# Kernel optimization log

Measured on AMD Instinct MI355X. Metric: run time of the kernel, lower is better.

The kernel has to match this reference:

```python
import jax, jax.numpy as jnp
import numpy as np

INNER_DIM = 64
NEG = 1e12


def _rotate_half_interleaved(x):
    # stack([-x[..., 1::2], x[..., ::2]], -1).reshape(x.shape)
    x2 = jnp.stack([-x[..., 1::2], x[..., ::2]], axis=-1)
    return x2.reshape(x.shape)


def setup_inputs() -> dict:
    key = jax.random.key(0)
    k1, k2 = jax.random.split(key)
    B, S, H = 16, 512, 768
    T, D = 9, INNER_DIM
    hidden = jax.random.normal(k1, (B, S, H), dtype=jnp.float32)
    W = jax.random.normal(k2, (H, T * 2 * D), dtype=jnp.float32) * 0.02
    b = jnp.zeros((T * 2 * D,), dtype=jnp.float32)
    attention_mask = jnp.ones((B, S), dtype=jnp.int32)
    return {"hidden": hidden, "W": W, "b": b, "attention_mask": attention_mask}


def reference(hidden, W, b, attention_mask):
    B, S, H = hidden.shape
    D = INNER_DIM
    T = W.shape[1] // (2 * D)

    # dense + split into per-type q/k: [B, S, T, 2D]
    out = (jnp.einsum('bsh,hc->bsc', hidden, W) + b).reshape(B, S, T, 2 * D)
    qw, kw = out[..., :D], out[..., D:]

    # inline sinusoidal RoPE (interleaved sin/cos layout)
    pos = jnp.arange(S, dtype=jnp.float32)[:, None]            # [S, 1]
    inv = jnp.power(10000.0, -2.0 * jnp.arange(D // 2, dtype=jnp.float32) / D)
    ang = pos * inv                                            # [S, D/2]
    cos_pos = jnp.repeat(jnp.cos(ang), 2, axis=-1)[None, :, None, :]  # [1,S,1,D]
    sin_pos = jnp.repeat(jnp.sin(ang), 2, axis=-1)[None, :, None, :]
    qw = qw * cos_pos + _rotate_half_interleaved(qw) * sin_pos
    kw = kw * cos_pos + _rotate_half_interleaved(kw) * sin_pos

    # pairwise scores per entity type: [B, T, S, S]
    logits = jnp.einsum('bmtd,bntd->btmn', qw, kw)

    # padding mask (key dim only, as in original expand) with large negative
    pm = attention_mask.astype(logits.dtype)[:, None, None, :]  # [B,1,1,S]
    logits = logits * pm - (1.0 - pm) * NEG

    # strict lower-triangular mask (only upper-triangular spans valid)
    tril = jnp.tril(jnp.ones((S, S), dtype=logits.dtype), -1)
    logits = logits - tril * NEG

    return logits / np.sqrt(D).astype(np.float32)
```

## Files before the change

kernel.cpp:

```cpp
#include <hip/hip_runtime.h>
#include <cstdint>
#include <cstddef>

#define NEG_C 1000000000000.0f

typedef __bf16 bf16x8 __attribute__((ext_vector_type(8)));
typedef float f32x4 __attribute__((ext_vector_type(4)));

union Frag {
    int4 i;
    bf16x8 b;
};

__device__ __forceinline__ unsigned short f32_to_bf16_rne(float f) {
    unsigned int u = __float_as_uint(f);
    u += 0x7fffu + ((u >> 16) & 1u);
    return (unsigned short)(u >> 16);
}

__device__ __forceinline__ void async_copy16(const void* g, void* l) {
    __builtin_amdgcn_global_load_lds(
        (const __attribute__((address_space(1))) unsigned int*)(uintptr_t)g,
        (__attribute__((address_space(3))) unsigned int*)(uintptr_t)l,
        16, 0, 0);
}

__global__ void prep_kernel(const float* __restrict__ W,
                            unsigned short* __restrict__ WT,
                            const float* __restrict__ hidden,
                            unsigned short* __restrict__ Ah) {
    __shared__ unsigned short tile[32][33];
    int blk = blockIdx.x;
    if (blk < 864) {
        int bx = blk % 36;
        int by = blk / 36;
        int x = threadIdx.x & 31;
        int y0 = threadIdx.x >> 5;
#pragma unroll
        for (int yy = 0; yy < 32; yy += 8) {
            int k = by * 32 + y0 + yy;
            int n = bx * 32 + x;
            tile[y0 + yy][x] = f32_to_bf16_rne(W[(size_t)k * 1152 + n]);
        }
        __syncthreads();
#pragma unroll
        for (int yy = 0; yy < 32; yy += 8) {
            int n = bx * 32 + y0 + yy;
            int k = by * 32 + x;
            WT[(size_t)n * 768 + k] = tile[x][y0 + yy];
        }
    } else {
        int idx = (blk - 864) * 256 + threadIdx.x;
        float4 v = ((const float4*)hidden)[idx];
        ushort4 o;
        o.x = f32_to_bf16_rne(v.x);
        o.y = f32_to_bf16_rne(v.y);
        o.z = f32_to_bf16_rne(v.z);
        o.w = f32_to_bf16_rne(v.w);
        ((ushort4*)Ah)[idx] = o;
    }
}

__global__ __launch_bounds__(256, 3) void gemm1_kernel(
    const unsigned short* __restrict__ Ah, const unsigned short* __restrict__ WT,
    const float* __restrict__ bias, unsigned short* __restrict__ proj) {
    const int K = 768, N = 1152;
    __shared__ unsigned short As[128 * 64];
    __shared__ unsigned short Bs[128 * 64];
    int tid = threadIdx.x;
    int lane = tid & 63;
    int wave = tid >> 6;
    int bm = blockIdx.y * 128;
    int bn = blockIdx.x * 128;
    int wm = (wave & 1) * 64;
    int wn = (wave >> 1) * 64;
    int col_l = lane & 15;
    int qg = lane >> 4;

    int c0 = wave * 4 * 64 + lane;
    f32x4 acc[4][4] = {};

    for (int k0 = 0; k0 < K; k0 += 64) {
        __syncthreads();
#pragma unroll
        for (int q = 0; q < 4; ++q) {
            int c = c0 + q * 64;
            int r = c >> 3;
            int g = (c & 7) ^ (r & 7);
            async_copy16(Ah + (size_t)(bm + r) * K + k0 + g * 8,
                         As + (size_t)(wave * 4 + q) * 512);
            async_copy16(WT + (size_t)(bn + r) * K + k0 + g * 8,
                         Bs + (size_t)(wave * 4 + q) * 512);
        }
        __syncthreads();
#pragma unroll
        for (int ks = 0; ks < 2; ++ks) {
            Frag qf[4], kf[4];
            int g = ks * 4 + qg;
#pragma unroll
            for (int i = 0; i < 4; ++i) {
                int rm = wm + i * 16 + col_l;
                int rn = wn + i * 16 + col_l;
                qf[i].i = *(const int4*)(As + rm * 64 + ((g ^ (rm & 7)) * 8));
                kf[i].i = *(const int4*)(Bs + rn * 64 + ((g ^ (rn & 7)) * 8));
            }
#pragma unroll
            for (int i = 0; i < 4; ++i)
#pragma unroll
                for (int j = 0; j < 4; ++j)
                    acc[i][j] = __builtin_amdgcn_mfma_f32_16x16x32_bf16(
                        kf[i].b, qf[j].b, acc[i][j], 0, 0, 0);
        }
    }

#pragma unroll
    for (int i = 0; i < 4; ++i) {
        int cn0 = wn + i * 16 + qg * 4;
        int gn0 = bn + cn0;
        float4 bb = *(const float4*)(bias + gn0);
        int p0 = (cn0 & 63) >> 1;
        float inv0 = exp2f(-0.41524101186091903f * (float)p0);
        float inv1 = exp2f(-0.41524101186091903f * (float)(p0 + 1));
#pragma unroll
        for (int j = 0; j < 4; ++j) {
            int gm = bm + wm + j * 16 + col_l;
            float s = (float)(gm & 511);
            float a0 = s * inv0, a1 = s * inv1;
            float sn0 = __sinf(a0), cs0 = __cosf(a0);
            float sn1 = __sinf(a1), cs1 = __cosf(a1);
            float v0 = acc[i][j][0] + bb.x;
            float v1 = acc[i][j][1] + bb.y;
            float v2 = acc[i][j][2] + bb.z;
            float v3 = acc[i][j][3] + bb.w;
            ushort4 o;
            o.x = f32_to_bf16_rne(v0 * cs0 - v1 * sn0);
            o.y = f32_to_bf16_rne(v1 * cs0 + v0 * sn0);
            o.z = f32_to_bf16_rne(v2 * cs1 - v3 * sn1);
            o.w = f32_to_bf16_rne(v3 * cs1 + v2 * sn1);
            *(ushort4*)(proj + (size_t)gm * N + gn0) = o;
        }
    }
}

__global__ __launch_bounds__(256, 3) void gemm2_kernel(
    const unsigned short* __restrict__ proj, const int* __restrict__ mask,
    float* __restrict__ out) {
    __shared__ unsigned short Qs[128 * 64];
    __shared__ unsigned short Ks[128 * 64];
    int bid = blockIdx.x;
    int batch = bid >> 4;
    int tl = bid & 15;
    int tm = tl >> 2, tn = tl & 3;
    int b = batch / 9, t = batch - b * 9;
    int tid = threadIdx.x, lane = tid & 63, wave = tid >> 6;
    int wm = (wave & 1) * 64, wn = (wave >> 1) * 64;
    int col_l = lane & 15;
    int qg = lane >> 4;
    size_t out_base = ((size_t)b * 9 + t) * 512 * 512;

    if (tm > tn) {
#pragma unroll 4
        for (int r = 0; r < 128; r += 8) {
            int row = r + (tid >> 5);
            int c4 = (tid & 31) * 4;
            int gm = tm * 128 + row;
            int gn = tn * 128 + c4;
            int4 mi = *(const int4*)(mask + b * 512 + gn);
            f32x4 v;
            v[0] = (-(1.0f - (float)mi.x) * NEG_C - NEG_C) * 0.125f;
            v[1] = (-(1.0f - (float)mi.y) * NEG_C - NEG_C) * 0.125f;
            v[2] = (-(1.0f - (float)mi.z) * NEG_C - NEG_C) * 0.125f;
            v[3] = (-(1.0f - (float)mi.w) * NEG_C - NEG_C) * 0.125f;
            *(f32x4*)(out + out_base + (size_t)gm * 512 + gn) = v;
        }
        return;
    }

    const unsigned short* qbase = proj + (((size_t)(b * 512 + tm * 128) * 9) + t) * 128;
    const unsigned short* kbase = proj + (((size_t)(b * 512 + tn * 128) * 9) + t) * 128 + 64;
#pragma unroll
    for (int q = 0; q < 4; ++q) {
        int c = (wave * 4 + q) * 64 + lane;
        int r = c >> 3;
        int g = (c & 7) ^ (r & 7);
        async_copy16(qbase + (size_t)r * 1152 + g * 8,
                     Qs + (size_t)(wave * 4 + q) * 512);
        async_copy16(kbase + (size_t)r * 1152 + g * 8,
                     Ks + (size_t)(wave * 4 + q) * 512);
    }
    __syncthreads();

    f32x4 acc[4][4] = {};
#pragma unroll
    for (int ks = 0; ks < 2; ++ks) {
        Frag qf[4], kf[4];
        int g = ks * 4 + qg;
#pragma unroll
        for (int i = 0; i < 4; ++i) {
            int rm = wm + i * 16 + col_l;
            int rn = wn + i * 16 + col_l;
            qf[i].i = *(const int4*)(Qs + rm * 64 + ((g ^ (rm & 7)) * 8));
            kf[i].i = *(const int4*)(Ks + rn * 64 + ((g ^ (rn & 7)) * 8));
        }
#pragma unroll
        for (int i = 0; i < 4; ++i)
#pragma unroll
            for (int j = 0; j < 4; ++j)
                acc[i][j] = __builtin_amdgcn_mfma_f32_16x16x32_bf16(
                    kf[i].b, qf[j].b, acc[i][j], 0, 0, 0);
    }

#pragma unroll
    for (int i = 0; i < 4; ++i) {
        int gn0 = tn * 128 + wn + i * 16 + qg * 4;
        int4 mi = *(const int4*)(mask + b * 512 + gn0);
#pragma unroll
        for (int j = 0; j < 4; ++j) {
            int gm = tm * 128 + wm + j * 16 + col_l;
            f32x4 v;
#pragma unroll
            for (int r = 0; r < 4; ++r) {
                float pm = (float)((&mi.x)[r]);
                float x = acc[i][j][r] * pm - (1.0f - pm) * NEG_C;
                if (gm > gn0 + r) x -= NEG_C;
                v[r] = x * 0.125f;
            }
            *(f32x4*)(out + out_base + (size_t)gm * 512 + gn0) = v;
        }
    }
}

extern "C" void kernel_launch(void* const* d_in, const int* in_sizes, int n_in,
                              void* d_out, int out_size, void* d_ws, size_t ws_size,
                              hipStream_t stream) {
    const float* hidden = (const float*)d_in[0];
    const float* W      = (const float*)d_in[1];
    const float* bias   = (const float*)d_in[2];
    const int*   mask   = (const int*)d_in[3];
    float* out = (float*)d_out;

    char* ws = (char*)d_ws;
    unsigned short* Ah   = (unsigned short*)(ws);
    unsigned short* WT   = (unsigned short*)(ws + 12582912);
    unsigned short* proj = (unsigned short*)(ws + 14352384);

    prep_kernel<<<7008, 256, 0, stream>>>(W, WT, hidden, Ah);
    dim3 g1(9, 64);
    gemm1_kernel<<<g1, 256, 0, stream>>>(Ah, WT, bias, proj);
    gemm2_kernel<<<2304, 256, 0, stream>>>(proj, mask, out);
}
```

Before: 214.3 us.

## Process a full row band per block with double-buffered K tiles in gemm2

gemm2 now launches one block per (batch, type, row tile). Each block loops over the upper-triangular column tiles, reusing the loaded Q tile and prefetching the next K tile into a second LDS buffer. The block also writes the masked lower-triangular tiles itself. This reduces the block count and redundant Q loads and overlaps K loads with MFMA work. The cost is uneven per-block work and fewer blocks in flight for a write-bound kernel.

```diff
diff --git a/kernel.cpp b/kernel.cpp
--- a/kernel.cpp
+++ b/kernel.cpp
@@ -146,24 +146,96 @@
     const unsigned short* __restrict__ proj, const int* __restrict__ mask,
     float* __restrict__ out) {
     __shared__ unsigned short Qs[128 * 64];
-    __shared__ unsigned short Ks[128 * 64];
+    __shared__ unsigned short Ks[2][128 * 64];
     int bid = blockIdx.x;
-    int batch = bid >> 4;
-    int tl = bid & 15;
-    int tm = tl >> 2, tn = tl & 3;
+    int tm = bid & 3;
+    int batch = bid >> 2;
     int b = batch / 9, t = batch - b * 9;
     int tid = threadIdx.x, lane = tid & 63, wave = tid >> 6;
     int wm = (wave & 1) * 64, wn = (wave >> 1) * 64;
     int col_l = lane & 15;
     int qg = lane >> 4;
-    size_t out_base = ((size_t)b * 9 + t) * 512 * 512;
-
-    if (tm > tn) {
-#pragma unroll 4
-        for (int r = 0; r < 128; r += 8) {
-            int row = r + (tid >> 5);
-            int c4 = (tid & 31) * 4;
-            int gm = tm * 128 + row;
+    size_t out_base = ((size_t)b * 9 + t) * (512 * 512);
+
+    {
+        const unsigned short* qbase =
+            proj + (((size_t)(b * 512 + tm * 128) * 9) + t) * 128;
+        const unsigned short* kbase = qbase + 64;
+#pragma unroll
+        for (int q = 0; q < 4; ++q) {
+            int c = (wave * 4 + q) * 64 + lane;
+            int r = c >> 3;
+            int g = (c & 7) ^ (r & 7);
+            async_copy16(qbase + (size_t)r * 1152 + g * 8,
+                         Qs + (size_t)(wave * 4 + q) * 512);
+            async_copy16(kbase + (size_t)r * 1152 + g * 8,
+                         Ks[0] + (size_t)(wave * 4 + q) * 512);
+        }
+    }
+    __syncthreads();
+
+    int cur = 0;
+    for (int tn = tm; tn < 4; ++tn) {
+        if (tn + 1 < 4) {
+            const unsigned short* kbase =
+                proj + (((size_t)(b * 512 + (tn + 1) * 128) * 9) + t) * 128 + 64;
+#pragma unroll
+            for (int q = 0; q < 4; ++q) {
+                int c = (wave * 4 + q) * 64 + lane;
+                int r = c >> 3;
+                int g = (c & 7) ^ (r & 7);
+                async_copy16(kbase + (size_t)r * 1152 + g * 8,
+                             Ks[cur ^ 1] + (size_t)(wave * 4 + q) * 512);
+            }
+        }
+
+        f32x4 acc[4][4] = {};
+#pragma unroll
+        for (int ks = 0; ks < 2; ++ks) {
+            Frag qf[4], kf[4];
+            int g = ks * 4 + qg;
+#pragma unroll
+            for (int i = 0; i < 4; ++i) {
+                int rm = wm + i * 16 + col_l;
+                int rn = wn + i * 16 + col_l;
+                qf[i].i = *(const int4*)(Qs + rm * 64 + ((g ^ (rm & 7)) * 8));
+                kf[i].i = *(const int4*)(Ks[cur] + rn * 64 + ((g ^ (rn & 7)) * 8));
+            }
+#pragma unroll
+            for (int i = 0; i < 4; ++i)
+#pragma unroll
+                for (int j = 0; j < 4; ++j)
+                    acc[i][j] = __builtin_amdgcn_mfma_f32_16x16x32_bf16(
+                        kf[i].b, qf[j].b, acc[i][j], 0, 0, 0);
+        }
+
+#pragma unroll
+        for (int i = 0; i < 4; ++i) {
+            int gn0 = tn * 128 + wn + i * 16 + qg * 4;
+            int4 mi = *(const int4*)(mask + b * 512 + gn0);
+#pragma unroll
+            for (int j = 0; j < 4; ++j) {
+                int gm = tm * 128 + wm + j * 16 + col_l;
+                f32x4 v;
+#pragma unroll
+                for (int r = 0; r < 4; ++r) {
+                    float pm = (float)((&mi.x)[r]);
+                    float x = acc[i][j][r] * pm - (1.0f - pm) * NEG_C;
+                    if (gm > gn0 + r) x -= NEG_C;
+                    v[r] = x * 0.125f;
+                }
+                *(f32x4*)(out + out_base + (size_t)gm * 512 + gn0) = v;
+            }
+        }
+
+        __syncthreads();
+        cur ^= 1;
+    }
+
+    {
+        int row = tid >> 5;
+        int c4 = (tid & 31) * 4;
+        for (int tn = 0; tn < tm; ++tn) {
             int gn = tn * 128 + c4;
             int4 mi = *(const int4*)(mask + b * 512 + gn);
             f32x4 v;
@@ -171,61 +243,11 @@
             v[1] = (-(1.0f - (float)mi.y) * NEG_C - NEG_C) * 0.125f;
             v[2] = (-(1.0f - (float)mi.z) * NEG_C - NEG_C) * 0.125f;
             v[3] = (-(1.0f - (float)mi.w) * NEG_C - NEG_C) * 0.125f;
-            *(f32x4*)(out + out_base + (size_t)gm * 512 + gn) = v;
-        }
-        return;
-    }
-
-    const unsigned short* qbase = proj + (((size_t)(b * 512 + tm * 128) * 9) + t) * 128;
-    const unsigned short* kbase = proj + (((size_t)(b * 512 + tn * 128) * 9) + t) * 128 + 64;
-#pragma unroll
-    for (int q = 0; q < 4; ++q) {
-        int c = (wave * 4 + q) * 64 + lane;
-        int r = c >> 3;
-        int g = (c & 7) ^ (r & 7);
-        async_copy16(qbase + (size_t)r * 1152 + g * 8,
-                     Qs + (size_t)(wave * 4 + q) * 512);
-        async_copy16(kbase + (size_t)r * 1152 + g * 8,
-                     Ks + (size_t)(wave * 4 + q) * 512);
-    }
-    __syncthreads();
-
-    f32x4 acc[4][4] = {};
-#pragma unroll
-    for (int ks = 0; ks < 2; ++ks) {
-        Frag qf[4], kf[4];
-        int g = ks * 4 + qg;
-#pragma unroll
-        for (int i = 0; i < 4; ++i) {
-            int rm = wm + i * 16 + col_l;
-            int rn = wn + i * 16 + col_l;
-            qf[i].i = *(const int4*)(Qs + rm * 64 + ((g ^ (rm & 7)) * 8));
-            kf[i].i = *(const int4*)(Ks + rn * 64 + ((g ^ (rn & 7)) * 8));
-        }
-#pragma unroll
-        for (int i = 0; i < 4; ++i)
-#pragma unroll
-            for (int j = 0; j < 4; ++j)
-                acc[i][j] = __builtin_amdgcn_mfma_f32_16x16x32_bf16(
-                    kf[i].b, qf[j].b, acc[i][j], 0, 0, 0);
-    }
-
-#pragma unroll
-    for (int i = 0; i < 4; ++i) {
-        int gn0 = tn * 128 + wn + i * 16 + qg * 4;
-        int4 mi = *(const int4*)(mask + b * 512 + gn0);
-#pragma unroll
-        for (int j = 0; j < 4; ++j) {
-            int gm = tm * 128 + wm + j * 16 + col_l;
-            f32x4 v;
-#pragma unroll
-            for (int r = 0; r < 4; ++r) {
-                float pm = (float)((&mi.x)[r]);
-                float x = acc[i][j][r] * pm - (1.0f - pm) * NEG_C;
-                if (gm > gn0 + r) x -= NEG_C;
-                v[r] = x * 0.125f;
-            }
-            *(f32x4*)(out + out_base + (size_t)gm * 512 + gn0) = v;
+#pragma unroll
+            for (int r8 = 0; r8 < 128; r8 += 8) {
+                int gm = tm * 128 + r8 + row;
+                *(f32x4*)(out + out_base + (size_t)gm * 512 + gn) = v;
+            }
         }
     }
 }
@@ -247,5 +269,5 @@
     prep_kernel<<<7008, 256, 0, stream>>>(W, WT, hidden, Ah);
     dim3 g1(9, 64);
     gemm1_kernel<<<g1, 256, 0, stream>>>(Ah, WT, bias, proj);
-    gemm2_kernel<<<2304, 256, 0, stream>>>(proj, mask, out);
-}
+    gemm2_kernel<<<576, 256, 0, stream>>>(proj, mask, out);
+}
```

New measurement: 224.4 us. +4.7%, slower.

## Double-buffer LDS tiles in projection GEMM to overlap loads with MFMA

Applied to the files above, without the earlier changes.

Gives the first GEMM two LDS buffers per operand and issues the async global-to-LDS copies for the next K slice before computing on the current one. This is meant to hide global load latency behind the MFMA work and removes one barrier per iteration. In exchange LDS use doubles to 64 KB per block and the occupancy hint drops from 3 to 2 blocks per CU. The gemm1 stage is only part of total time, which is dominated by the large fp32 output write in gemm2.

```diff
diff --git a/kernel.cpp b/kernel.cpp
--- a/kernel.cpp
+++ b/kernel.cpp
@@ -61,12 +61,12 @@
     }
 }
 
-__global__ __launch_bounds__(256, 3) void gemm1_kernel(
+__global__ __launch_bounds__(256, 2) void gemm1_kernel(
     const unsigned short* __restrict__ Ah, const unsigned short* __restrict__ WT,
     const float* __restrict__ bias, unsigned short* __restrict__ proj) {
     const int K = 768, N = 1152;
-    __shared__ unsigned short As[128 * 64];
-    __shared__ unsigned short Bs[128 * 64];
+    __shared__ unsigned short As[2][128 * 64];
+    __shared__ unsigned short Bs[2][128 * 64];
     int tid = threadIdx.x;
     int lane = tid & 63;
     int wave = tid >> 6;
@@ -80,38 +80,57 @@
     int c0 = wave * 4 * 64 + lane;
     f32x4 acc[4][4] = {};
 
-    for (int k0 = 0; k0 < K; k0 += 64) {
+    int sr[4], sg[4];
+#pragma unroll
+    for (int q = 0; q < 4; ++q) {
+        int c = c0 + q * 64;
+        sr[q] = c >> 3;
+        sg[q] = (c & 7) ^ (sr[q] & 7);
+    }
+
+#define STAGE(buf, k0)                                                        \
+    _Pragma("unroll")                                                         \
+    for (int q = 0; q < 4; ++q) {                                             \
+        async_copy16(Ah + (size_t)(bm + sr[q]) * K + (k0) + sg[q] * 8,        \
+                     &As[buf][(wave * 4 + q) * 512]);                         \
+        async_copy16(WT + (size_t)(bn + sr[q]) * K + (k0) + sg[q] * 8,        \
+                     &Bs[buf][(wave * 4 + q) * 512]);                         \
+    }
+
+#define COMPUTE(buf)                                                          \
+    _Pragma("unroll")                                                         \
+    for (int ks = 0; ks < 2; ++ks) {                                          \
+        Frag qf[4], kf[4];                                                    \
+        int g = ks * 4 + qg;                                                  \
+        _Pragma("unroll")                                                     \
+        for (int i = 0; i < 4; ++i) {                                         \
+            int rm = wm + i * 16 + col_l;                                     \
+            int rn = wn + i * 16 + col_l;                                     \
+            qf[i].i = *(const int4*)(&As[buf][rm * 64 + ((g ^ (rm & 7)) * 8)]); \
+            kf[i].i = *(const int4*)(&Bs[buf][rn * 64 + ((g ^ (rn & 7)) * 8)]); \
+        }                                                                     \
+        _Pragma("unroll")                                                     \
+        for (int i = 0; i < 4; ++i)                                           \
+            _Pragma("unroll")                                                 \
+            for (int j = 0; j < 4; ++j)                                       \
+                acc[i][j] = __builtin_amdgcn_mfma_f32_16x16x32_bf16(          \
+                    kf[i].b, qf[j].b, acc[i][j], 0, 0, 0);                    \
+    }
+
+    STAGE(0, 0)
+    __syncthreads();
+
+    int cur = 0;
+    for (int k0 = 64; k0 < K; k0 += 64) {
+        STAGE(cur ^ 1, k0)
+        COMPUTE(cur)
         __syncthreads();
-#pragma unroll
-        for (int q = 0; q < 4; ++q) {
-            int c = c0 + q * 64;
-            int r = c >> 3;
-            int g = (c & 7) ^ (r & 7);
-            async_copy16(Ah + (size_t)(bm + r) * K + k0 + g * 8,
-                         As + (size_t)(wave * 4 + q) * 512);
-            async_copy16(WT + (size_t)(bn + r) * K + k0 + g * 8,
-                         Bs + (size_t)(wave * 4 + q) * 512);
-        }
-        __syncthreads();
-#pragma unroll
-        for (int ks = 0; ks < 2; ++ks) {
-            Frag qf[4], kf[4];
-            int g = ks * 4 + qg;
-#pragma unroll
-            for (int i = 0; i < 4; ++i) {
-                int rm = wm + i * 16 + col_l;
-                int rn = wn + i * 16 + col_l;
-                qf[i].i = *(const int4*)(As + rm * 64 + ((g ^ (rm & 7)) * 8));
-                kf[i].i = *(const int4*)(Bs + rn * 64 + ((g ^ (rn & 7)) * 8));
-            }
-#pragma unroll
-            for (int i = 0; i < 4; ++i)
-#pragma unroll
-                for (int j = 0; j < 4; ++j)
-                    acc[i][j] = __builtin_amdgcn_mfma_f32_16x16x32_bf16(
-                        kf[i].b, qf[j].b, acc[i][j], 0, 0, 0);
-        }
-    }
+        cur ^= 1;
+    }
+    COMPUTE(cur)
+
+#undef STAGE
+#undef COMPUTE
 
 #pragma unroll
     for (int i = 0; i < 4; ++i) {
```

After: 217.3 us. About the same (+1.4%).
